# Performance work log

Measured on AMD Instinct MI355X. Metric: run time of the kernel, lower is better.

The kernel has to match this reference:

```python
import jax, jax.numpy as jnp
import numpy as np

B, S, E, H = 2, 2048, 1024, 16
D = E // H  # head dim = 64
MAX_REL = 512


def setup_inputs() -> dict:
    key = jax.random.key(0)
    ks = jax.random.split(key, 12)
    w = 1.0 / np.sqrt(E)
    return {
        "query": jax.random.normal(ks[0], (B, S, E), jnp.float32),
        "key": jax.random.normal(ks[1], (B, S, E), jnp.float32),
        "value": jax.random.normal(ks[2], (B, S, E), jnp.float32),
        "Wq": jax.random.normal(ks[3], (E, E), jnp.float32) * w,
        "bq": jax.random.normal(ks[4], (E,), jnp.float32) * 0.02,
        "Wk": jax.random.normal(ks[5], (E, E), jnp.float32) * w,
        "bk": jax.random.normal(ks[6], (E,), jnp.float32) * 0.02,
        "Wv": jax.random.normal(ks[7], (E, E), jnp.float32) * w,
        "bv": jax.random.normal(ks[8], (E,), jnp.float32) * 0.02,
        "Wo": jax.random.normal(ks[9], (E, E), jnp.float32) * w,
        "bo": jax.random.normal(ks[10], (E,), jnp.float32) * 0.02,
        "rel_bias_table": jax.random.normal(ks[11], (2 * MAX_REL + 1, H), jnp.float32),
    }


def _rel_bias(rel_bias_table, sq, sk):
    # clamped relative positions -> [Sq, Sk] indices into table
    rel = jnp.arange(sq)[:, None] - jnp.arange(sk)[None, :]
    rel = jnp.clip(rel, -MAX_REL, MAX_REL) + MAX_REL
    bias = rel_bias_table[rel]                 # [Sq, Sk, H]
    return jnp.transpose(bias, (2, 0, 1))[None]  # [1, H, Sq, Sk]


def reference(query, key, value, Wq, bq, Wk, bk, Wv, bv, Wo, bo, rel_bias_table):
    b, sq, e = query.shape
    sk = key.shape[1]
    scale = D ** -0.5
    # projections (torch Linear: x @ W.T + b), split heads -> [B, H, S, D]
    q = (query @ Wq.T + bq).reshape(b, sq, H, D).transpose(0, 2, 1, 3)
    k = (key @ Wk.T + bk).reshape(b, sk, H, D).transpose(0, 2, 1, 3)
    v = (value @ Wv.T + bv).reshape(b, sk, H, D).transpose(0, 2, 1, 3)
    scores = jnp.einsum("bhqd,bhkd->bhqk", q, k) * scale
    scores = scores + _rel_bias(rel_bias_table, sq, sk)
    # causal mask (causal_mask=True branch)
    causal = jnp.arange(sk)[None, :] > jnp.arange(sq)[:, None]
    scores = jnp.where(causal[None, None], -jnp.inf, scores)
    attn = jax.nn.softmax(scores, axis=-1)
    out = jnp.einsum("bhqk,bhkd->bhqd", attn, v)
    out = out.transpose(0, 2, 1, 3).reshape(b, sq, e)
    out = out @ Wo.T + bo
    return out, attn
```

## Files before the change

### kernel.cpp

```cpp
#include <hip/hip_runtime.h>
#include <hip/hip_bf16.h>
#include <stdint.h>

#define Sx 2048
#define Ex 1024
#define Hx 16
#define Dx 64

typedef __attribute__((ext_vector_type(8))) short short8;
typedef __attribute__((ext_vector_type(4))) short bh4;
typedef __attribute__((ext_vector_type(4))) float f32x4;
typedef __attribute__((ext_vector_type(2))) unsigned int u32x2;

__device__ inline short f2bf(float f) {
    unsigned u = __builtin_bit_cast(unsigned, f);
    u = (u + 0x7fffu + ((u >> 16) & 1u)) >> 16;
    return (short)u;
}

__device__ inline unsigned cvtpk_bf16(float a, float b) {
    unsigned r;
    asm("v_cvt_pk_bf16_f32 %0, %1, %2" : "=v"(r) : "v"(a), "v"(b));
    return r;
}

__device__ inline float exp2fast(float x) { return __builtin_amdgcn_exp2f(x); }

__device__ inline void gload16(const short* g, short* l) {
    __builtin_amdgcn_global_load_lds((const __attribute__((address_space(1))) void*)g,
                                     (__attribute__((address_space(3))) void*)l, 16, 0, 0);
}

__global__ __launch_bounds__(256) void prep(const float* __restrict__ q,
                                            const float* __restrict__ k,
                                            const float* __restrict__ v,
                                            const float* __restrict__ wq,
                                            const float* __restrict__ wk,
                                            const float* __restrict__ wv_,
                                            const float* __restrict__ wo,
                                            short* __restrict__ ws) {
    const int seg = blockIdx.y;
    const float* src; size_t n, doff;
    switch (seg) {
        case 0: src = q;   n = 4194304; doff = 0;        break;
        case 1: src = k;   n = 4194304; doff = 4194304;  break;
        case 2: src = v;   n = 4194304; doff = 8388608;  break;
        case 3: src = wq;  n = 1048576; doff = 12582912; break;
        case 4: src = wk;  n = 1048576; doff = 13631488; break;
        case 5: src = wv_; n = 1048576; doff = 14680064; break;
        default: src = wo; n = 1048576; doff = 15728640; break;
    }
    short* dst = ws + doff;
    for (size_t i = ((size_t)blockIdx.x * 256 + threadIdx.x) * 8; i < n;
         i += (size_t)gridDim.x * 256 * 8) {
        float4 f0 = *(const float4*)&src[i];
        float4 f1 = *(const float4*)&src[i + 4];
        short8 s;
        s[0]=f2bf(f0.x); s[1]=f2bf(f0.y); s[2]=f2bf(f0.z); s[3]=f2bf(f0.w);
        s[4]=f2bf(f1.x); s[5]=f2bf(f1.y); s[6]=f2bf(f1.z); s[7]=f2bf(f1.w);
        *(short8*)&dst[i] = s;
    }
}

__global__ __launch_bounds__(256) void gemm_qkv3(const short* __restrict__ wsb,
                                                 const float* __restrict__ bq,
                                                 const float* __restrict__ bk,
                                                 const float* __restrict__ bv,
                                                 short* __restrict__ qh,
                                                 short* __restrict__ kh,
                                                 short* __restrict__ vt) {
    __shared__ short wt[128 * 64];
    __shared__ short xt[128 * 64];
    const int z = blockIdx.z;
    const short* X  = wsb + (size_t)z * 4194304;
    const short* Wm = wsb + 12582912 + (size_t)z * 1048576;
    const float* bias = (z == 0) ? bq : (z == 1) ? bk : bv;
    short* outb = (z == 0) ? qh : (z == 1) ? kh : vt;
    const bool vmode = (z == 2);

    const int tid = threadIdx.x;
    const int l = tid & 63, wv = tid >> 6;
    const int r15 = l & 15, g = l >> 4;
    const int wm = wv >> 1, wn = wv & 1;
    const int i0 = blockIdx.x << 7;
    const int j0 = blockIdx.y << 7;
    const int lrow = l >> 3, lgi = l & 7;

    f32x4 acc[4][4] = {};

    for (int k0 = 0; k0 < Ex; k0 += 64) {
        __syncthreads();
        #pragma unroll
        for (int p = 0; p < 4; ++p) {
            int row = p * 32 + wv * 8 + lrow;
            int col = ((lgi ^ (row & 7)) << 3) + k0;
            gload16(&Wm[(size_t)(j0 + row) * Ex + col], &wt[(p * 32 + wv * 8) * 64]);
            gload16(&X [(size_t)(i0 + row) * Ex + col], &xt[(p * 32 + wv * 8) * 64]);
        }
        __syncthreads();
        const short* At = vmode ? xt : wt;
        const short* Bt = vmode ? wt : xt;
        #pragma unroll
        for (int kk = 0; kk < 64; kk += 32) {
            const int sw = (((kk >> 3) + g) ^ (r15 & 7)) << 3;
            short8 a[4], b[4];
            #pragma unroll
            for (int m = 0; m < 4; ++m)
                a[m] = *(const short8*)&At[(wm * 64 + m * 16 + r15) * 64 + sw];
            #pragma unroll
            for (int n = 0; n < 4; ++n)
                b[n] = *(const short8*)&Bt[(wn * 64 + n * 16 + r15) * 64 + sw];
            #pragma unroll
            for (int m = 0; m < 4; ++m)
                #pragma unroll
                for (int n = 0; n < 4; ++n)
                    acc[m][n] = __builtin_amdgcn_mfma_f32_16x16x32_bf16(a[m], b[n], acc[m][n], 0, 0, 0);
        }
    }

    if (!vmode) {
        #pragma unroll
        for (int m = 0; m < 4; ++m) {
            int jb = j0 + wm * 64 + m * 16 + (g << 2);
            float4 bvv = *(const float4*)&bias[jb];
            #pragma unroll
            for (int n = 0; n < 4; ++n) {
                int i = i0 + wn * 64 + n * 16 + r15;
                bh4 s;
                s[0] = f2bf(acc[m][n][0] + bvv.x);
                s[1] = f2bf(acc[m][n][1] + bvv.y);
                s[2] = f2bf(acc[m][n][2] + bvv.z);
                s[3] = f2bf(acc[m][n][3] + bvv.w);
                *(bh4*)&outb[(size_t)i * Ex + jb] = s;
            }
        }
    } else {
        #pragma unroll
        for (int m = 0; m < 4; ++m) {
            int ib = i0 + wm * 64 + m * 16 + (g << 2);
            int b_ = ib >> 11, s0 = ib & 2047;
            #pragma unroll
            for (int n = 0; n < 4; ++n) {
                int j = j0 + wn * 64 + n * 16 + r15;
                float bj = bias[j];
                bh4 s;
                s[0] = f2bf(acc[m][n][0] + bj);
                s[1] = f2bf(acc[m][n][1] + bj);
                s[2] = f2bf(acc[m][n][2] + bj);
                s[3] = f2bf(acc[m][n][3] + bj);
                *(bh4*)&outb[((size_t)(b_ * Hx + (j >> 6)) * Dx + (j & 63)) * Sx + s0] = s;
            }
        }
    }
}

__global__ __launch_bounds__(256) void gemm_out(const short* __restrict__ Xb,
                                                const short* __restrict__ Wb,
                                                const float* __restrict__ bias,
                                                float* __restrict__ out) {
    __shared__ short wt[2][128 * 64];
    __shared__ short xt[2][128 * 64];
    const int tid = threadIdx.x;
    const int l = tid & 63, wv = tid >> 6;
    const int r15 = l & 15, g = l >> 4;
    const int wm = wv >> 1, wn = wv & 1;
    const int i0 = blockIdx.x << 7;
    const int j0 = blockIdx.y << 7;
    const int lrow = l >> 3, lgi = l & 7;

    f32x4 acc[4][4] = {};

    auto stage = [&](int it, int buf) {
        int k0 = it << 6;
        #pragma unroll
        for (int p = 0; p < 4; ++p) {
            int row = p * 32 + wv * 8 + lrow;
            int col = ((lgi ^ (row & 7)) << 3) + k0;
            gload16(&Wb[(size_t)(j0 + row) * Ex + col], &wt[buf][(p * 32 + wv * 8) * 64]);
            gload16(&Xb[(size_t)(i0 + row) * Ex + col], &xt[buf][(p * 32 + wv * 8) * 64]);
        }
    };

    stage(0, 0);
    for (int it = 0; it < 16; ++it) {
        __syncthreads();
        if (it + 1 < 16) stage(it + 1, (it + 1) & 1);
        const int cur = it & 1;
        #pragma unroll
        for (int kk = 0; kk < 64; kk += 32) {
            const int sw = (((kk >> 3) + g) ^ (r15 & 7)) << 3;
            short8 a[4], b[4];
            #pragma unroll
            for (int m = 0; m < 4; ++m)
                a[m] = *(const short8*)&wt[cur][(wm * 64 + m * 16 + r15) * 64 + sw];
            #pragma unroll
            for (int n = 0; n < 4; ++n)
                b[n] = *(const short8*)&xt[cur][(wn * 64 + n * 16 + r15) * 64 + sw];
            #pragma unroll
            for (int m = 0; m < 4; ++m)
                #pragma unroll
                for (int n = 0; n < 4; ++n)
                    acc[m][n] = __builtin_amdgcn_mfma_f32_16x16x32_bf16(a[m], b[n], acc[m][n], 0, 0, 0);
        }
    }

    #pragma unroll
    for (int m = 0; m < 4; ++m) {
        int jb = j0 + wm * 64 + m * 16 + (g << 2);
        float4 bvv = *(const float4*)&bias[jb];
        #pragma unroll
        for (int n = 0; n < 4; ++n) {
            int i = i0 + wn * 64 + n * 16 + r15;
            float4 o;
            o.x = acc[m][n][0] + bvv.x;
            o.y = acc[m][n][1] + bvv.y;
            o.z = acc[m][n][2] + bvv.z;
            o.w = acc[m][n][3] + bvv.w;
            *(float4*)&out[(size_t)i * Ex + jb] = o;
        }
    }
}

__global__ void attn_fused(const short* __restrict__ qhat,
                           const short* __restrict__ khat,
                           const short* __restrict__ vT,
                           const float* __restrict__ table,
                           float* __restrict__ attn,
                           short* __restrict__ om) {
    __shared__ short ks[2][64 * 64];
    __shared__ short vs[2][64 * 64];
    __shared__ short ps[128 * 64];
    __shared__ float bl[1028];

    const int tid = threadIdx.x;
    const int l = tid & 63, wv = tid >> 6;
    const int r15 = l & 15, g = l >> 4;

    const int lin = blockIdx.x + (blockIdx.y << 4);
    const int xcd = lin & 7, slot = lin >> 3;
    const int bh = xcd + ((slot & 3) << 3);
    const int qidx = (slot >> 2) & 7;
    const int qt = (slot >> 5) ? (15 - qidx) : qidx;

    const int b = bh >> 4, h = bh & 15;
    const int lrow = l >> 3, lgi = l & 7;
    const int nkt = 2 * qt + 2;
    const float cs2 = 0.18033688f;

    for (int i = tid; i < 1025; i += 512)
        bl[i] = (i < 512) ? -3e30f : (table[i * Hx + h] - 16.0f) * 1.4426950408889634f;

    short8 qf[2];
    {
        const size_t qrow = (size_t)(b * Sx + (qt << 7) + wv * 16 + r15);
        #pragma unroll
        for (int kk = 0; kk < 2; ++kk)
            qf[kk] = *(const short8*)&qhat[qrow * Ex + h * Dx + kk * 32 + g * 8];
    }

    auto stageK = [&](int kt, int buf) {
        int row = wv * 8 + lrow;
        gload16(&khat[(size_t)(b * Sx + (kt << 6) + row) * Ex + h * Dx + ((lgi ^ (row & 7)) << 3)],
                &ks[buf][(wv * 8) * 64]);
    };
    auto stageV = [&](int kt, int buf) {
        int row = wv * 8 + lrow;
        gload16(&vT[((size_t)bh * Dx + row) * Sx + (kt << 6) + ((lgi ^ (row & 7)) << 3)],
                &vs[buf][(wv * 8) * 64]);
    };

    float sr = 0.f;
    const int qg0 = (qt << 7) + wv * 16 + r15;

    stageK(0, 0);
    for (int kt = 0; kt < nkt; ++kt) {
        __syncthreads();
        if (kt + 1 < nkt) stageK(kt + 1, (kt + 1) & 1);
        const int cur = kt & 1;
        f32x4 sf[4] = {};
        __builtin_amdgcn_s_setprio(1);
        #pragma unroll
        for (int kk = 0; kk < 64; kk += 32) {
            const int sw = (((kk >> 3) + g) ^ (r15 & 7)) << 3;
            short8 a[4];
            #pragma unroll
            for (int m = 0; m < 4; ++m) a[m] = *(const short8*)&ks[cur][(m * 16 + r15) * 64 + sw];
            #pragma unroll
            for (int m = 0; m < 4; ++m)
                sf[m] = __builtin_amdgcn_mfma_f32_16x16x32_bf16(a[m], qf[kk >> 5], sf[m], 0, 0, 0);
        }
        __builtin_amdgcn_s_setprio(0);
        const int kcb = (kt << 6) + (g << 2);
        int base = qg0 + 512 - kcb;
        float psum = 0.f;
        #pragma unroll
        for (int m = 0; m < 4; ++m) {
            int b0 = base - m * 16;
            #pragma unroll
            for (int r = 0; r < 4; ++r) {
                int idx = b0 - r;
                idx = idx > 1024 ? 1024 : idx;
                psum += exp2fast(fmaf(sf[m][r], cs2, bl[idx]));
            }
        }
        psum += __shfl_xor(psum, 16);
        psum += __shfl_xor(psum, 32);
        sr += psum;
    }

    const float inv = 1.0f / sr;
    f32x4 of[4] = {};
    float* Ap = attn + (size_t)bh * ((size_t)Sx * Sx);

    __syncthreads();
    stageK(0, 0);
    stageV(0, 0);
    for (int kt = 0; kt < nkt; ++kt) {
        __syncthreads();
        if (kt + 1 < nkt) { stageK(kt + 1, (kt + 1) & 1); stageV(kt + 1, (kt + 1) & 1); }
        const int cur = kt & 1;
        f32x4 sf[4] = {};
        __builtin_amdgcn_s_setprio(1);
        #pragma unroll
        for (int kk = 0; kk < 64; kk += 32) {
            const int sw = (((kk >> 3) + g) ^ (r15 & 7)) << 3;
            short8 a[4];
            #pragma unroll
            for (int m = 0; m < 4; ++m) a[m] = *(const short8*)&ks[cur][(m * 16 + r15) * 64 + sw];
            #pragma unroll
            for (int m = 0; m < 4; ++m)
                sf[m] = __builtin_amdgcn_mfma_f32_16x16x32_bf16(a[m], qf[kk >> 5], sf[m], 0, 0, 0);
        }
        __builtin_amdgcn_s_setprio(0);
        {
            const int q = qg0;
            const int qrow = wv * 16 + r15;
            #pragma unroll
            for (int m = 0; m < 4; ++m) {
                int kc0 = (kt << 6) + m * 16 + (g << 2);
                int b0 = q + 512 - kc0;
                f32x4 pv;
                #pragma unroll
                for (int r = 0; r < 4; ++r) {
                    int idx = b0 - r;
                    idx = idx > 1024 ? 1024 : idx;
                    pv[r] = exp2fast(fmaf(sf[m][r], cs2, bl[idx])) * inv;
                }
                __builtin_nontemporal_store(pv, (f32x4*)&Ap[(size_t)q * Sx + kc0]);
                u32x2 pk;
                pk[0] = cvtpk_bf16(pv[0], pv[1]);
                pk[1] = cvtpk_bf16(pv[2], pv[3]);
                int gphys = (m * 2 + (g >> 1)) ^ (r15 & 7);
                *(u32x2*)&ps[qrow * 64 + gphys * 8 + (g & 1) * 4] = pk;
            }
        }
        __builtin_amdgcn_s_setprio(1);
        #pragma unroll
        for (int kk = 0; kk < 64; kk += 32) {
            const int sw = (((kk >> 3) + g) ^ (r15 & 7)) << 3;
            short8 a[4], bp;
            #pragma unroll
            for (int m = 0; m < 4; ++m) a[m] = *(const short8*)&vs[cur][(m * 16 + r15) * 64 + sw];
            bp = *(const short8*)&ps[(wv * 16 + r15) * 64 + sw];
            #pragma unroll
            for (int m = 0; m < 4; ++m)
                of[m] = __builtin_amdgcn_mfma_f32_16x16x32_bf16(a[m], bp, of[m], 0, 0, 0);
        }
        __builtin_amdgcn_s_setprio(0);
    }

    {
        const int qv = (qt << 7) + wv * 16 + r15;
        #pragma unroll
        for (int m = 0; m < 4; ++m) {
            int d0 = m * 16 + (g << 2);
            u32x2 s;
            s[0] = cvtpk_bf16(of[m][0], of[m][1]);
            s[1] = cvtpk_bf16(of[m][2], of[m][3]);
            *(u32x2*)&om[(size_t)(b * Sx + qv) * Ex + h * Dx + d0] = s;
        }
    }

    const int c0 = nkt << 6;
    f32x4 z = {0.f, 0.f, 0.f, 0.f};
    for (int row = tid >> 3; row < 128; row += 64) {
        size_t base = (size_t)((qt << 7) + row) * Sx;
        for (int c = c0 + ((tid & 7) << 2); c < Sx; c += 32)
            __builtin_nontemporal_store(z, (f32x4*)&Ap[base + c]);
    }
}

extern "C" void kernel_launch(void* const* d_in, const int* in_sizes, int n_in,
                              void* d_out, int out_size, void* d_ws, size_t ws_size,
                              hipStream_t stream) {
    const float* query = (const float*)d_in[0];
    const float* key   = (const float*)d_in[1];
    const float* value = (const float*)d_in[2];
    const float* bq = (const float*)d_in[4];
    const float* bk = (const float*)d_in[6];
    const float* bv = (const float*)d_in[8];
    const float* bo = (const float*)d_in[10];
    const float* Wq = (const float*)d_in[3];
    const float* Wk = (const float*)d_in[5];
    const float* Wv = (const float*)d_in[7];
    const float* Wo = (const float*)d_in[9];
    const float* tbl = (const float*)d_in[11];

    short* ws = (short*)d_ws;
    short* qx  = ws;
    short* wob = ws + 15728640;
    short* qh  = ws + 16777216;
    short* kh  = ws + 20971520;
    short* vt  = ws + 25165824;

    float* outp  = (float*)d_out;
    float* attnp = outp + 4194304;

    prep<<<dim3(1024, 7), 256, 0, stream>>>(query, key, value, Wq, Wk, Wv, Wo, ws);
    gemm_qkv3<<<dim3(32, 8, 3), 256, 0, stream>>>(ws, bq, bk, bv, qh, kh, vt);
    attn_fused<<<dim3(16, 32), 512, 0, stream>>>(qh, kh, vt, tbl, attnp, qx);
    gemm_out<<<dim3(32, 8), 256, 0, stream>>>(qx, wob, bo, outp);
}
```

Baseline: 273.7 us.

## Write attention probabilities from double-buffered LDS tile as coalesced rows

Attention probabilities are no longer stored straight from MFMA fragments. The bf16 P tile is kept in a double-buffered LDS array and written to global memory one iteration later as coalesced row-major float4 stores, which hides the writes behind the next tile's compute. The goal is better coalescing of the large attn output and overlap of that traffic with compute. In exchange, the attn output now holds bf16-rounded values instead of full fp32, which costs precision, and the extra LDS buffer may lower occupancy.

```diff
diff --git a/kernel.cpp b/kernel.cpp
--- a/kernel.cpp
+++ b/kernel.cpp
@@ -229,7 +229,7 @@
                            short* __restrict__ om) {
     __shared__ short ks[2][64 * 64];
     __shared__ short vs[2][64 * 64];
-    __shared__ short ps[128 * 64];
+    __shared__ short ps[2][128 * 64];
     __shared__ float bl[1028];
 
     const int tid = threadIdx.x;
@@ -276,7 +276,7 @@
     for (int kt = 0; kt < nkt; ++kt) {
         __syncthreads();
         if (kt + 1 < nkt) stageK(kt + 1, (kt + 1) & 1);
-        const int cur = kt & 1;
+        const short* kb = ks[kt & 1];
         f32x4 sf[4] = {};
         __builtin_amdgcn_s_setprio(1);
         #pragma unroll
@@ -284,7 +284,7 @@
             const int sw = (((kk >> 3) + g) ^ (r15 & 7)) << 3;
             short8 a[4];
             #pragma unroll
-            for (int m = 0; m < 4; ++m) a[m] = *(const short8*)&ks[cur][(m * 16 + r15) * 64 + sw];
+            for (int m = 0; m < 4; ++m) a[m] = *(const short8*)&kb[(m * 16 + r15) * 64 + sw];
             #pragma unroll
             for (int m = 0; m < 4; ++m)
                 sf[m] = __builtin_amdgcn_mfma_f32_16x16x32_bf16(a[m], qf[kk >> 5], sf[m], 0, 0, 0);
@@ -312,12 +312,27 @@
     f32x4 of[4] = {};
     float* Ap = attn + (size_t)bh * ((size_t)Sx * Sx);
 
+    auto bulk_store = [&](int t) {
+        const short* pb = ps[t & 1];
+        const int j2 = tid & 15;
+        int row = tid >> 4;
+        #pragma unroll
+        for (int h2 = 0; h2 < 4; ++h2, row += 32) {
+            bh4 v = *(const bh4*)&pb[row * 64 + (((j2 >> 1) ^ (row & 7)) << 3) + (j2 & 1) * 4];
+            f32x4 o;
+            #pragma unroll
+            for (int r = 0; r < 4; ++r)
+                o[r] = __builtin_bit_cast(float, (unsigned)((unsigned short)v[r]) << 16);
+            __builtin_nontemporal_store(o, (f32x4*)&Ap[(size_t)((qt << 7) + row) * Sx + (t << 6) + j2 * 4]);
+        }
+    };
+
     __syncthreads();
-    stageK(0, 0);
-    stageV(0, 0);
+    stageK(0, 0); stageV(0, 0);
     for (int kt = 0; kt < nkt; ++kt) {
         __syncthreads();
         if (kt + 1 < nkt) { stageK(kt + 1, (kt + 1) & 1); stageV(kt + 1, (kt + 1) & 1); }
+        if (kt > 0) bulk_store(kt - 1);
         const int cur = kt & 1;
         f32x4 sf[4] = {};
         __builtin_amdgcn_s_setprio(1);
@@ -333,25 +348,28 @@
         }
         __builtin_amdgcn_s_setprio(0);
         {
-            const int q = qg0;
             const int qrow = wv * 16 + r15;
+            short* pw = ps[cur];
             #pragma unroll
             for (int m = 0; m < 4; ++m) {
                 int kc0 = (kt << 6) + m * 16 + (g << 2);
-                int b0 = q + 512 - kc0;
-                f32x4 pv;
-                #pragma unroll
-                for (int r = 0; r < 4; ++r) {
-                    int idx = b0 - r;
-                    idx = idx > 1024 ? 1024 : idx;
-                    pv[r] = exp2fast(fmaf(sf[m][r], cs2, bl[idx])) * inv;
+                int b0 = qg0 + 512 - kc0;
+                float pv0, pv1, pv2, pv3;
+                {
+                    int i0_ = b0;     i0_ = i0_ > 1024 ? 1024 : i0_;
+                    int i1_ = b0 - 1; i1_ = i1_ > 1024 ? 1024 : i1_;
+                    int i2_ = b0 - 2; i2_ = i2_ > 1024 ? 1024 : i2_;
+                    int i3_ = b0 - 3; i3_ = i3_ > 1024 ? 1024 : i3_;
+                    pv0 = exp2fast(fmaf(sf[m][0], cs2, bl[i0_])) * inv;
+                    pv1 = exp2fast(fmaf(sf[m][1], cs2, bl[i1_])) * inv;
+                    pv2 = exp2fast(fmaf(sf[m][2], cs2, bl[i2_])) * inv;
+                    pv3 = exp2fast(fmaf(sf[m][3], cs2, bl[i3_])) * inv;
                 }
-                __builtin_nontemporal_store(pv, (f32x4*)&Ap[(size_t)q * Sx + kc0]);
                 u32x2 pk;
-                pk[0] = cvtpk_bf16(pv[0], pv[1]);
-                pk[1] = cvtpk_bf16(pv[2], pv[3]);
+                pk[0] = cvtpk_bf16(pv0, pv1);
+                pk[1] = cvtpk_bf16(pv2, pv3);
                 int gphys = (m * 2 + (g >> 1)) ^ (r15 & 7);
-                *(u32x2*)&ps[qrow * 64 + gphys * 8 + (g & 1) * 4] = pk;
+                *(u32x2*)&pw[qrow * 64 + gphys * 8 + (g & 1) * 4] = pk;
             }
         }
         __builtin_amdgcn_s_setprio(1);
@@ -361,13 +379,15 @@
             short8 a[4], bp;
             #pragma unroll
             for (int m = 0; m < 4; ++m) a[m] = *(const short8*)&vs[cur][(m * 16 + r15) * 64 + sw];
-            bp = *(const short8*)&ps[(wv * 16 + r15) * 64 + sw];
+            bp = *(const short8*)&ps[cur][(wv * 16 + r15) * 64 + sw];
             #pragma unroll
             for (int m = 0; m < 4; ++m)
                 of[m] = __builtin_amdgcn_mfma_f32_16x16x32_bf16(a[m], bp, of[m], 0, 0, 0);
         }
         __builtin_amdgcn_s_setprio(0);
     }
+    __syncthreads();
+    bulk_store(nkt - 1);
 
     {
         const int qv = (qt << 7) + wv * 16 + r15;
```

After: 224.0 us, median of 2. 18.1% less time.
